# Optimization experiments

Hardware: AMD Instinct MI355X
Metric: run time of the kernel (lower is better)

The kernel has to match this reference:

```python
import jax, jax.numpy as jnp
import numpy as np
import math

EMBED = 1024
HEADS = 16
HEAD_DIM = EMBED // HEADS
FF = 4096
LAYERS = 4
BATCH = 2
SEQ = 2048
EPS = 1e-5
ADAPTIVE = True
MAX_LENGTH = 2048


def setup_inputs() -> dict:
    key = jax.random.key(0)
    ks = jax.random.split(key, 20)
    s = 0.02
    inp = {
        "x": jax.random.normal(ks[0], (BATCH, SEQ, EMBED), jnp.float32),
        # per-layer stacked parameters, torch Linear convention W:[out,in]
        "Wq": jax.random.normal(ks[1], (LAYERS, EMBED, EMBED)) * s,
        "bq": jnp.zeros((LAYERS, EMBED)),
        "Wk": jax.random.normal(ks[2], (LAYERS, EMBED, EMBED)) * s,
        "bk": jnp.zeros((LAYERS, EMBED)),
        "Wv": jax.random.normal(ks[3], (LAYERS, EMBED, EMBED)) * s,
        "bv": jnp.zeros((LAYERS, EMBED)),
        "Wo": jax.random.normal(ks[4], (LAYERS, EMBED, EMBED)) * s,
        "bo": jnp.zeros((LAYERS, EMBED)),
        "W1": jax.random.normal(ks[5], (LAYERS, FF, EMBED)) * s,
        "b1": jnp.zeros((LAYERS, FF)),
        "W2": jax.random.normal(ks[6], (LAYERS, EMBED, FF)) * s,
        "b2": jnp.zeros((LAYERS, EMBED)),
        "g1": jnp.ones((LAYERS, EMBED)),
        "be1": jnp.zeros((LAYERS, EMBED)),
        "g2": jnp.ones((LAYERS, EMBED)),
        "be2": jnp.zeros((LAYERS, EMBED)),
    }
    return inp


def _layer_norm(x, g, b):
    mu = jnp.mean(x, axis=-1, keepdims=True)
    var = jnp.mean(jnp.square(x - mu), axis=-1, keepdims=True)
    return (x - mu) * jax.lax.rsqrt(var + EPS) * g + b


def _band_mask(seq_len):
    # adaptive, length-dependent sparse band: window ~ sqrt(seq_len)
    w = int(math.ceil(math.sqrt(seq_len))) if ADAPTIVE else MAX_LENGTH
    idx = jnp.arange(seq_len)
    return jnp.abs(idx[:, None] - idx[None, :]) <= w  # [S,S] bool


def _sparse_attn(x, Wq, bq, Wk, bk, Wv, bv, Wo, bo, band):
    B, S, E = x.shape
    def proj(W, b):
        return (x @ W.T + b).reshape(B, S, HEADS, HEAD_DIM)
    q = proj(Wq, bq)
    k = proj(Wk, bk)
    v = proj(Wv, bv)
    scores = jnp.einsum("bshd,bthd->bhst", q, k) / math.sqrt(HEAD_DIM)
    scores = jnp.where(band[None, None], scores, jnp.float32(-1e9))
    attn = jax.nn.softmax(scores, axis=-1)
    out = jnp.einsum("bhst,bthd->bshd", attn, v).reshape(B, S, E)
    return out @ Wo.T + bo


def reference(x, Wq, bq, Wk, bk, Wv, bv, Wo, bo, W1, b1, W2, b2, g1, be1, g2, be2):
    band = _band_mask(x.shape[1])
    for i in range(LAYERS):
        attn = _sparse_attn(x, Wq[i], bq[i], Wk[i], bk[i], Wv[i], bv[i],
                            Wo[i], bo[i], band)
        x = _layer_norm(x + attn, g1[i], be1[i])
        ff = jax.nn.relu(x @ W1[i].T + b1[i]) @ W2[i].T + b2[i]
        x = _layer_norm(x + ff, g2[i], be2[i])
    return x  # dropout is identity in eval mode
```

## Files before the change

### kernel.cpp

```cpp
#include <hip/hip_runtime.h>
#include <hip/hip_bf16.h>

using bf16 = __hip_bfloat16;
typedef __bf16 bf16x8v __attribute__((ext_vector_type(8)));
typedef __bf16 bf16x4v __attribute__((ext_vector_type(4)));
typedef float f32x4v __attribute__((ext_vector_type(4)));

#define EMBED 1024
#define FF_DIM 4096
#define NTOK 4096
#define SEQL 2048
#define HD 64
#define WBAND 46
#define LN_EPS 1e-5f

__device__ __forceinline__ void gload16(const bf16* g, bf16* l)
{
  __builtin_amdgcn_global_load_lds(
      (const __attribute__((address_space(1))) void*)g,
      (__attribute__((address_space(3))) void*)l, 16, 0, 0);
}

__global__ __launch_bounds__(256) void detect_dtype(
    const unsigned int* __restrict__ xw, int* __restrict__ flag)
{
  __shared__ int votes[256];
  int v = 0;
#pragma unroll
  for (int j = 0; j < 4; j++) {
    unsigned int w = xw[1 + threadIdx.x * 4 + j];
    unsigned int e = (w >> 7) & 0xFFu;
    v += (e == 0u || (e >= 0x58u && e <= 0x88u)) ? 1 : 0;
  }
  votes[threadIdx.x] = v;
  __syncthreads();
  if (threadIdx.x == 0) {
    int s = 0;
    for (int i = 0; i < 256; i++) s += votes[i];
    *flag = (s > 512) ? 1 : 0;
  }
}

__global__ __launch_bounds__(256) void cast_param(
    const void* __restrict__ src, bf16* __restrict__ dst, int n,
    const int* __restrict__ dflag)
{
  const int is_bf16 = *dflag;
  for (int i = blockIdx.x * 256 + threadIdx.x; i < n; i += gridDim.x * 256)
    dst[i] = is_bf16 ? ((const bf16*)src)[i] : (bf16)(((const float*)src)[i]);
}

__global__ __launch_bounds__(256) void cast_in(
    const void* __restrict__ x, float* __restrict__ xf,
    bf16* __restrict__ xb, int n, const int* __restrict__ dflag)
{
  const int is_bf16 = *dflag;
  const int i = blockIdx.x * 256 + threadIdx.x;
  if (i < n) {
    float v = is_bf16 ? (float)((const bf16*)x)[i] : ((const float*)x)[i];
    xf[i] = v;
    xb[i] = (bf16)v;
  }
}

__global__ __launch_bounds__(256) void cast_weights(
    const void* __restrict__ wq, const void* __restrict__ wk,
    const void* __restrict__ wv, const void* __restrict__ wo,
    const void* __restrict__ w1, const void* __restrict__ w2,
    size_t off_ee, size_t off_fe, bf16* __restrict__ dst,
    const int* __restrict__ dflag)
{
  const int is_bf16 = *dflag;
  const int c = blockIdx.x * 256 + threadIdx.x;
  const size_t i = (size_t)c * 8;
  const void* src;
  size_t si;
  if (i < 4194304) {
    const int t = (int)(i >> 20);
    src = (t == 0) ? wq : (t == 1) ? wk : (t == 2) ? wv : wo;
    si  = off_ee + (i & 1048575);
  } else if (i < 8388608) { src = w1; si = off_fe + (i - 4194304); }
  else                    { src = w2; si = off_fe + (i - 8388608); }
  bf16x8v o;
  if (is_bf16) {
    o = *reinterpret_cast<const bf16x8v*>((const bf16*)src + si);
  } else {
    f32x4v a = *reinterpret_cast<const f32x4v*>((const float*)src + si);
    f32x4v b = *reinterpret_cast<const f32x4v*>((const float*)src + si + 4);
#pragma unroll
    for (int j = 0; j < 4; j++) { o[j] = (__bf16)a[j]; o[j + 4] = (__bf16)b[j]; }
  }
  *reinterpret_cast<bf16x8v*>(dst + i) = o;
}

template<int EPI, int BN>
__device__ __forceinline__ void gemm_core(
    const bf16* __restrict__ A, const bf16* __restrict__ W,
    const bf16* __restrict__ bias, bf16* __restrict__ C,
    int N, int K, int row0, int col0W, int col0C)
{
  __shared__ __align__(16) bf16 lA[128 * 32];
  __shared__ __align__(16) bf16 lB[BN * 32];
  constexpr int NJ = BN / 32;

  const int tid  = threadIdx.x;
  const int wave = tid >> 6;
  const int lane = tid & 63;
  const int wr0  = (wave >> 1) * 64;
  const int wc0  = (wave & 1) * (BN / 2);

  f32x4v acc[4][NJ];
#pragma unroll
  for (int i = 0; i < 4; i++)
#pragma unroll
    for (int j = 0; j < NJ; j++) acc[i][j] = (f32x4v){0.f, 0.f, 0.f, 0.f};

  const int srow = wave * 16 + (lane >> 2);
  const int skc  = (lane & 3) * 8;
  const bf16* Ag = A + (size_t)(row0 + srow) * K + skc;
  const bf16* Bg;
  if constexpr (BN == 128) Bg = W + (size_t)(col0W + srow) * K + skc;
  else                     Bg = W + (size_t)(col0W + (tid >> 2)) * K + (size_t)(tid & 3) * 8;
  bf16* lAp = lA + tid * 8;
  bf16* lBp = lB + tid * 8;

  const int fr = lane & 15;
  const int q8 = (lane >> 4) * 8;

  for (int k0 = 0; k0 < K; k0 += 32) {
    __syncthreads();
    gload16(Ag + k0, lAp);
    gload16(Ag + (size_t)64 * K + k0, lAp + 2048);
    gload16(Bg + k0, lBp);
    if constexpr (BN == 128)
      gload16(Bg + (size_t)64 * K + k0, lBp + 2048);
    __syncthreads();

    bf16x8v af[4], bw[NJ];
#pragma unroll
    for (int i = 0; i < 4; i++)
      af[i] = *reinterpret_cast<const bf16x8v*>(&lA[(wr0 + i * 16 + fr) * 32 + q8]);
#pragma unroll
    for (int j = 0; j < NJ; j++)
      bw[j] = *reinterpret_cast<const bf16x8v*>(&lB[(wc0 + j * 16 + fr) * 32 + q8]);
#pragma unroll
    for (int i = 0; i < 4; i++)
#pragma unroll
      for (int j = 0; j < NJ; j++)
        acc[i][j] = __builtin_amdgcn_mfma_f32_16x16x32_bf16(af[i], bw[j], acc[i][j], 0, 0, 0);
  }

  const int quad = (lane >> 4) * 4;
#pragma unroll
  for (int j = 0; j < NJ; j++) {
    const int col = col0C + wc0 + j * 16 + fr;
    const float bvf = (float)bias[col];
#pragma unroll
    for (int i = 0; i < 4; i++) {
      const int r0 = row0 + wr0 + i * 16 + quad;
#pragma unroll
      for (int r = 0; r < 4; r++) {
        float v = acc[i][j][r] + bvf;
        if (EPI == 1) v = fmaxf(v, 0.f);
        C[(size_t)(r0 + r) * N + col] = (bf16)v;
      }
    }
  }
}

template<int EPI, int BN>
__global__ __launch_bounds__(256) void gemm_bt(
    const bf16* __restrict__ A, const bf16* __restrict__ W,
    const bf16* __restrict__ bias, bf16* __restrict__ C, int N, int K)
{
  gemm_core<EPI, BN>(A, W, bias, C, N, K,
                     blockIdx.x * 128, blockIdx.y * BN, blockIdx.y * BN);
}

__global__ __launch_bounds__(256) void gemm_qkv(
    const bf16* __restrict__ A, const bf16* __restrict__ Wqkv,
    const bf16* __restrict__ bq, const bf16* __restrict__ bk, const bf16* __restrict__ bv,
    bf16* __restrict__ Cq, bf16* __restrict__ Ck, bf16* __restrict__ Cv, int K)
{
  const int cg = blockIdx.y * 128;
  const int t  = cg >> 10;
  const bf16* bias = (t == 0) ? bq : (t == 1) ? bk : bv;
  bf16*       C    = (t == 0) ? Cq : (t == 1) ? Ck : Cv;
  gemm_core<0, 128>(A, Wqkv, bias, C, 1024, K,
                    blockIdx.x * 128, cg, cg & 1023);
}

#define SKI(t, d)  ((((t) * 64) + (d)) ^ (((t) & 7) << 3))
#define SVI(d, t)  ((((d) * 128) + (t)) ^ (((d) & 7) << 3))
#define SPI(q, c)  ((((q) * 128) + (c)) ^ (((q) & 7) << 3))
#define SSI(q, c)  ((((q) * 128) + (c)) ^ (((q) & 7) << 2))

__global__ __launch_bounds__(256) void attn_band(
    const bf16* __restrict__ Q, const bf16* __restrict__ Kp,
    const bf16* __restrict__ Vp, bf16* __restrict__ O)
{
  const int sblk = blockIdx.x;
  const int bh   = blockIdx.y;
  const int b    = bh >> 4;
  const int h    = bh & 15;
  const int s0   = sblk * 32;
  int tlo = s0 - WBAND;       if (tlo < 0) tlo = 0;
  int thi = s0 + 31 + WBAND;  if (thi > SEQL - 1) thi = SEQL - 1;
  const int L = thi - tlo + 1;

  __shared__ __align__(16) bf16  sQf[32 * 64];
  __shared__ __align__(16) bf16  sKf[128 * 64];
  __shared__ __align__(16) bf16  sVtf[64 * 128];
  __shared__ __align__(16) float sSf[32 * 128];
  __shared__ __align__(16) bf16  sPf[32 * 128];
  __shared__ float red1[32][8];
  __shared__ float red2[32][8];
  __shared__ float sInv[32];

  const int tid  = threadIdx.x;
  const int wave = tid >> 6;
  const int lane = tid & 63;
  const size_t base = ((size_t)b * SEQL) * EMBED + (size_t)h * HD;

  bf16x8v vz;
#pragma unroll
  for (int j = 0; j < 8; j++) vz[j] = (__bf16)0.f;

  {
    const int sl = tid >> 3, d0 = (tid & 7) * 8;
    *reinterpret_cast<bf16x8v*>(&sQf[SKI(sl, d0)]) =
        *reinterpret_cast<const bf16x8v*>(&Q[base + (size_t)(s0 + sl) * EMBED + d0]);
  }
  for (int i = tid; i < 128 * 8; i += 256) {
    const int tl = i >> 3, d0 = (i & 7) * 8;
    bf16x8v v = vz;
    if (tl < L)
      v = *reinterpret_cast<const bf16x8v*>(&Kp[base + (size_t)(tlo + tl) * EMBED + d0]);
    *reinterpret_cast<bf16x8v*>(&sKf[SKI(tl, d0)]) = v;
  }
  for (int i = tid; i < 128 * 8; i += 256) {
    const int tl = i & 127, d0 = ((i >> 7) & 7) * 8;
    bf16x8v v = vz;
    if (tl < L)
      v = *reinterpret_cast<const bf16x8v*>(&Vp[base + (size_t)(tlo + tl) * EMBED + d0]);
#pragma unroll
    for (int j = 0; j < 8; j++)
      sVtf[SVI(d0 + j, tl)] = reinterpret_cast<const bf16*>(&v)[j];
  }
  __syncthreads();

  const int fr   = lane & 15;
  const int q8   = (lane >> 4) * 8;
  const int quad = (lane >> 4) * 4;

  {
    f32x4v acc[2][2];
#pragma unroll
    for (int mi = 0; mi < 2; mi++)
#pragma unroll
      for (int nj = 0; nj < 2; nj++) acc[mi][nj] = (f32x4v){0.f, 0.f, 0.f, 0.f};
#pragma unroll
    for (int ks = 0; ks < 2; ks++) {
      bf16x8v a0 = *reinterpret_cast<const bf16x8v*>(&sQf[SKI(fr,      ks * 32 + q8)]);
      bf16x8v a1 = *reinterpret_cast<const bf16x8v*>(&sQf[SKI(16 + fr, ks * 32 + q8)]);
      bf16x8v b0 = *reinterpret_cast<const bf16x8v*>(&sKf[SKI((wave * 2    ) * 16 + fr, ks * 32 + q8)]);
      bf16x8v b1 = *reinterpret_cast<const bf16x8v*>(&sKf[SKI((wave * 2 + 1) * 16 + fr, ks * 32 + q8)]);
      acc[0][0] = __builtin_amdgcn_mfma_f32_16x16x32_bf16(a0, b0, acc[0][0], 0, 0, 0);
      acc[0][1] = __builtin_amdgcn_mfma_f32_16x16x32_bf16(a0, b1, acc[0][1], 0, 0, 0);
      acc[1][0] = __builtin_amdgcn_mfma_f32_16x16x32_bf16(a1, b0, acc[1][0], 0, 0, 0);
      acc[1][1] = __builtin_amdgcn_mfma_f32_16x16x32_bf16(a1, b1, acc[1][1], 0, 0, 0);
    }
#pragma unroll
    for (int nj = 0; nj < 2; nj++) {
      const int c = (wave * 2 + nj) * 16 + fr;
      const int t = tlo + c;
      const bool cvalid = (c < L);
#pragma unroll
      for (int mi = 0; mi < 2; mi++) {
#pragma unroll
        for (int r = 0; r < 4; r++) {
          const int row = mi * 16 + quad + r;
          int dd = (s0 + row) - t; if (dd < 0) dd = -dd;
          sSf[SSI(row, c)] = (cvalid && dd <= WBAND) ? acc[mi][nj][r] * 0.125f
                                                     : -1e30f;
        }
      }
    }
  }
  __syncthreads();

  const int sl   = tid & 31;
  const int part = tid >> 5;
  float pmax = -1e30f;
#pragma unroll
  for (int k = 0; k < 16; k++) pmax = fmaxf(pmax, sSf[SSI(sl, part + 8 * k)]);
  red1[sl][part] = pmax;
  __syncthreads();
  float rmax = red1[sl][0];
#pragma unroll
  for (int p = 1; p < 8; p++) rmax = fmaxf(rmax, red1[sl][p]);

  float psum = 0.f;
#pragma unroll
  for (int k = 0; k < 16; k++) {
    const int c = part + 8 * k;
    float e = __expf(sSf[SSI(sl, c)] - rmax);
    sPf[SPI(sl, c)] = (bf16)e;
    psum += e;
  }
  red2[sl][part] = psum;
  __syncthreads();
  float rsum = 0.f;
#pragma unroll
  for (int p = 0; p < 8; p++) rsum += red2[sl][p];
  if (part == 0) sInv[sl] = 1.f / rsum;
  __syncthreads();

  {
    const int mi = wave >> 1;
    const int nb = (wave & 1) * 2;
    f32x4v acc[2];
    acc[0] = (f32x4v){0.f, 0.f, 0.f, 0.f};
    acc[1] = (f32x4v){0.f, 0.f, 0.f, 0.f};
#pragma unroll
    for (int ks = 0; ks < 4; ks++) {
      bf16x8v a  = *reinterpret_cast<const bf16x8v*>(&sPf[SPI(mi * 16 + fr, ks * 32 + q8)]);
      bf16x8v b0 = *reinterpret_cast<const bf16x8v*>(&sVtf[SVI((nb    ) * 16 + fr, ks * 32 + q8)]);
      bf16x8v b1 = *reinterpret_cast<const bf16x8v*>(&sVtf[SVI((nb + 1) * 16 + fr, ks * 32 + q8)]);
      acc[0] = __builtin_amdgcn_mfma_f32_16x16x32_bf16(a, b0, acc[0], 0, 0, 0);
      acc[1] = __builtin_amdgcn_mfma_f32_16x16x32_bf16(a, b1, acc[1], 0, 0, 0);
    }
#pragma unroll
    for (int nj = 0; nj < 2; nj++) {
      const int d = (nb + nj) * 16 + fr;
#pragma unroll
      for (int r = 0; r < 4; r++) {
        const int row = mi * 16 + quad + r;
        O[base + (size_t)(s0 + row) * EMBED + d] = (bf16)(acc[nj][r] * sInv[row]);
      }
    }
  }
}

__global__ __launch_bounds__(256) void resid_ln(
    const float* xin, const bf16* __restrict__ y,
    const bf16* __restrict__ g, const bf16* __restrict__ be,
    float* xf_out, bf16* __restrict__ xb_out,
    void* __restrict__ final_out, const int* __restrict__ dflag)
{
  __shared__ float red1[4];
  __shared__ float red2[4];
  const int row = blockIdx.x;
  const int tid = threadIdx.x;
  const size_t base = (size_t)row * EMBED + (size_t)tid * 4;

  f32x4v  xv = *reinterpret_cast<const f32x4v*>(xin + base);
  bf16x4v yv = *reinterpret_cast<const bf16x4v*>(y + base);
  float v[4];
#pragma unroll
  for (int j = 0; j < 4; j++) v[j] = xv[j] + (float)yv[j];

  float s = v[0] + v[1] + v[2] + v[3];
#pragma unroll
  for (int off = 32; off > 0; off >>= 1) s += __shfl_down(s, off, 64);
  if ((tid & 63) == 0) red1[tid >> 6] = s;
  __syncthreads();
  const float mu = (red1[0] + red1[1] + red1[2] + red1[3]) * (1.f / EMBED);

  float sq = 0.f;
#pragma unroll
  for (int j = 0; j < 4; j++) { const float d = v[j] - mu; sq += d * d; }
#pragma unroll
  for (int off = 32; off > 0; off >>= 1) sq += __shfl_down(sq, off, 64);
  if ((tid & 63) == 0) red2[tid >> 6] = sq;
  __syncthreads();
  const float rstd = rsqrtf((red2[0] + red2[1] + red2[2] + red2[3]) * (1.f / EMBED) + LN_EPS);

  bf16x4v gv = *reinterpret_cast<const bf16x4v*>(g + (size_t)tid * 4);
  bf16x4v bv = *reinterpret_cast<const bf16x4v*>(be + (size_t)tid * 4);
  f32x4v of;
  bf16x4v ov;
#pragma unroll
  for (int j = 0; j < 4; j++) {
    of[j] = (v[j] - mu) * rstd * (float)gv[j] + (float)bv[j];
    ov[j] = (__bf16)of[j];
  }
  *reinterpret_cast<f32x4v*>(xf_out + base) = of;
  *reinterpret_cast<bf16x4v*>(xb_out + base) = ov;
  if (final_out) {
    if (*dflag)
      *reinterpret_cast<bf16x4v*>((bf16*)final_out + base) = ov;
    else
      *reinterpret_cast<f32x4v*>((float*)final_out + base) = of;
  }
}

extern "C" void kernel_launch(void* const* d_in, const int* in_sizes, int n_in,
                              void* d_out, int out_size, void* d_ws, size_t ws_size,
                              hipStream_t stream)
{
  char* ws = (char*)d_ws;
  const size_t MB = 1024 * 1024;
  int*   flag = (int*)ws;
  bf16*  pp   = (bf16*)(ws + 4096);
  float* xf   = (float*)(ws + 1 * MB);
  bf16*  xb   = (bf16*)(ws + 17 * MB);
  bf16*  q    = (bf16*)(ws + 25 * MB);
  bf16*  kk   = (bf16*)(ws + 33 * MB);
  bf16*  vv   = (bf16*)(ws + 41 * MB);
  bf16*  ao   = q;
  bf16*  hh   = (bf16*)(ws + 25 * MB);
  bf16*  y    = (bf16*)(ws + 57 * MB);
  bf16*  wbf  = (bf16*)(ws + 65 * MB);

  bf16* pbq = pp;            bf16* pbk = pp + 4096;  bf16* pbv = pp + 8192;
  bf16* pbo = pp + 12288;    bf16* pb1 = pp + 16384; bf16* pb2 = pp + 32768;
  bf16* pg1 = pp + 36864;    bf16* pe1 = pp + 40960;
  bf16* pg2 = pp + 45056;    bf16* pe2 = pp + 49152;

  detect_dtype<<<1, 256, 0, stream>>>((const unsigned int*)d_in[0], flag);

  cast_param<<<16, 256, 0, stream>>>(d_in[2],  pbq, 4096,  flag);
  cast_param<<<16, 256, 0, stream>>>(d_in[4],  pbk, 4096,  flag);
  cast_param<<<16, 256, 0, stream>>>(d_in[6],  pbv, 4096,  flag);
  cast_param<<<16, 256, 0, stream>>>(d_in[8],  pbo, 4096,  flag);
  cast_param<<<64, 256, 0, stream>>>(d_in[10], pb1, 16384, flag);
  cast_param<<<16, 256, 0, stream>>>(d_in[12], pb2, 4096,  flag);
  cast_param<<<16, 256, 0, stream>>>(d_in[13], pg1, 4096,  flag);
  cast_param<<<16, 256, 0, stream>>>(d_in[14], pe1, 4096,  flag);
  cast_param<<<16, 256, 0, stream>>>(d_in[15], pg2, 4096,  flag);
  cast_param<<<16, 256, 0, stream>>>(d_in[16], pe2, 4096,  flag);

  cast_in<<<dim3((NTOK * EMBED) / 256), 256, 0, stream>>>(
      d_in[0], xf, xb, NTOK * EMBED, flag);

  for (int l = 0; l < 4; l++) {
    cast_weights<<<6144, 256, 0, stream>>>(
        d_in[1], d_in[3], d_in[5], d_in[7], d_in[9], d_in[11],
        (size_t)l * 1048576, (size_t)l * 4194304, wbf, flag);

    gemm_qkv<<<dim3(32, 24), 256, 0, stream>>>(
        xb, wbf, pbq + l * 1024, pbk + l * 1024, pbv + l * 1024,
        q, kk, vv, EMBED);
    attn_band<<<dim3(SEQL / 32, 32), 256, 0, stream>>>(q, kk, vv, ao);
    gemm_bt<0, 64><<<dim3(32, 16), 256, 0, stream>>>(
        ao, wbf + 3 * 1048576, pbo + l * 1024, y, EMBED, EMBED);
    resid_ln<<<dim3(NTOK), 256, 0, stream>>>(xf, y, pg1 + l * 1024, pe1 + l * 1024, xf, xb, nullptr, flag);
    gemm_bt<1, 128><<<dim3(32, 32), 256, 0, stream>>>(
        xb, wbf + 4 * 1048576, pb1 + l * 4096, hh, FF_DIM, EMBED);
    gemm_bt<0, 64><<<dim3(32, 16), 256, 0, stream>>>(
        hh, wbf + 8 * 1048576, pb2 + l * 1024, y, EMBED, FF_DIM);
    resid_ln<<<dim3(NTOK), 256, 0, stream>>>(xf, y, pg2 + l * 1024, pe2 + l * 1024, xf, xb,
                                             l == 3 ? d_out : nullptr, flag);
  }
}
```

Before: 1.201 ms.

## Split-K the N=1024 output GEMMs into two partials summed in residual LayerNorm

```diff
diff --git a/kernel.cpp b/kernel.cpp
--- a/kernel.cpp
+++ b/kernel.cpp
@@ -97,7 +97,8 @@
 __device__ __forceinline__ void gemm_core(
     const bf16* __restrict__ A, const bf16* __restrict__ W,
     const bf16* __restrict__ bias, bf16* __restrict__ C,
-    int N, int K, int row0, int col0W, int col0C)
+    int N, int Kstride, int Kbeg, int Klen,
+    int row0, int col0W, int col0C)
 {
   __shared__ __align__(16) bf16 lA[128 * 32];
   __shared__ __align__(16) bf16 lB[BN * 32];
@@ -117,23 +118,25 @@
 
   const int srow = wave * 16 + (lane >> 2);
   const int skc  = (lane & 3) * 8;
-  const bf16* Ag = A + (size_t)(row0 + srow) * K + skc;
+  const bf16* Ag = A + (size_t)(row0 + srow) * Kstride + Kbeg + skc;
   const bf16* Bg;
-  if constexpr (BN == 128) Bg = W + (size_t)(col0W + srow) * K + skc;
-  else                     Bg = W + (size_t)(col0W + (tid >> 2)) * K + (size_t)(tid & 3) * 8;
+  if constexpr (BN == 128)
+    Bg = W + (size_t)(col0W + srow) * Kstride + Kbeg + skc;
+  else
+    Bg = W + (size_t)(col0W + (tid >> 2)) * Kstride + Kbeg + (size_t)(tid & 3) * 8;
   bf16* lAp = lA + tid * 8;
   bf16* lBp = lB + tid * 8;
 
   const int fr = lane & 15;
   const int q8 = (lane >> 4) * 8;
 
-  for (int k0 = 0; k0 < K; k0 += 32) {
+  for (int k0 = 0; k0 < Klen; k0 += 32) {
     __syncthreads();
     gload16(Ag + k0, lAp);
-    gload16(Ag + (size_t)64 * K + k0, lAp + 2048);
+    gload16(Ag + (size_t)64 * Kstride + k0, lAp + 2048);
     gload16(Bg + k0, lBp);
     if constexpr (BN == 128)
-      gload16(Bg + (size_t)64 * K + k0, lBp + 2048);
+      gload16(Bg + (size_t)64 * Kstride + k0, lBp + 2048);
     __syncthreads();
 
     bf16x8v af[4], bw[NJ];
@@ -154,7 +157,7 @@
 #pragma unroll
   for (int j = 0; j < NJ; j++) {
     const int col = col0C + wc0 + j * 16 + fr;
-    const float bvf = (float)bias[col];
+    const float bvf = bias ? (float)bias[col] : 0.f;
 #pragma unroll
     for (int i = 0; i < 4; i++) {
       const int r0 = row0 + wr0 + i * 16 + quad;
@@ -168,12 +171,16 @@
   }
 }
 
-template<int EPI, int BN>
+template<int EPI, int BN, int NS>
 __global__ __launch_bounds__(256) void gemm_bt(
     const bf16* __restrict__ A, const bf16* __restrict__ W,
-    const bf16* __restrict__ bias, bf16* __restrict__ C, int N, int K)
-{
-  gemm_core<EPI, BN>(A, W, bias, C, N, K,
+    const bf16* __restrict__ bias, bf16* __restrict__ C0, bf16* __restrict__ C1,
+    int N, int K)
+{
+  const int z  = (NS > 1) ? blockIdx.z : 0;
+  const int Kp = K / NS;
+  gemm_core<EPI, BN>(A, W, z == 0 ? bias : nullptr, z == 0 ? C0 : C1,
+                     N, K, z * Kp, Kp,
                      blockIdx.x * 128, blockIdx.y * BN, blockIdx.y * BN);
 }
 
@@ -186,7 +193,7 @@
   const int t  = cg >> 10;
   const bf16* bias = (t == 0) ? bq : (t == 1) ? bk : bv;
   bf16*       C    = (t == 0) ? Cq : (t == 1) ? Ck : Cv;
-  gemm_core<0, 128>(A, Wqkv, bias, C, 1024, K,
+  gemm_core<0, 128>(A, Wqkv, bias, C, 1024, K, 0, K,
                     blockIdx.x * 128, cg, cg & 1023);
 }
 
@@ -343,9 +350,9 @@
 }
 
 __global__ __launch_bounds__(256) void resid_ln(
-    const float* xin, const bf16* __restrict__ y,
+    const float* xin, const bf16* __restrict__ y0, const bf16* y1,
     const bf16* __restrict__ g, const bf16* __restrict__ be,
-    float* xf_out, bf16* __restrict__ xb_out,
+    float* xf_out, bf16* xb_out,
     void* __restrict__ final_out, const int* __restrict__ dflag)
 {
   __shared__ float red1[4];
@@ -354,11 +361,12 @@
   const int tid = threadIdx.x;
   const size_t base = (size_t)row * EMBED + (size_t)tid * 4;
 
-  f32x4v  xv = *reinterpret_cast<const f32x4v*>(xin + base);
-  bf16x4v yv = *reinterpret_cast<const bf16x4v*>(y + base);
+  f32x4v  xv  = *reinterpret_cast<const f32x4v*>(xin + base);
+  bf16x4v yv0 = *reinterpret_cast<const bf16x4v*>(y0 + base);
+  bf16x4v yv1 = *reinterpret_cast<const bf16x4v*>(y1 + base);
   float v[4];
 #pragma unroll
-  for (int j = 0; j < 4; j++) v[j] = xv[j] + (float)yv[j];
+  for (int j = 0; j < 4; j++) v[j] = xv[j] + (float)yv0[j] + (float)yv1[j];
 
   float s = v[0] + v[1] + v[2] + v[3];
 #pragma unroll
@@ -443,14 +451,16 @@
         xb, wbf, pbq + l * 1024, pbk + l * 1024, pbv + l * 1024,
         q, kk, vv, EMBED);
     attn_band<<<dim3(SEQL / 32, 32), 256, 0, stream>>>(q, kk, vv, ao);
-    gemm_bt<0, 64><<<dim3(32, 16), 256, 0, stream>>>(
-        ao, wbf + 3 * 1048576, pbo + l * 1024, y, EMBED, EMBED);
-    resid_ln<<<dim3(NTOK), 256, 0, stream>>>(xf, y, pg1 + l * 1024, pe1 + l * 1024, xf, xb, nullptr, flag);
-    gemm_bt<1, 128><<<dim3(32, 32), 256, 0, stream>>>(
-        xb, wbf + 4 * 1048576, pb1 + l * 4096, hh, FF_DIM, EMBED);
-    gemm_bt<0, 64><<<dim3(32, 16), 256, 0, stream>>>(
-        hh, wbf + 8 * 1048576, pb2 + l * 1024, y, EMBED, FF_DIM);
-    resid_ln<<<dim3(NTOK), 256, 0, stream>>>(xf, y, pg2 + l * 1024, pe2 + l * 1024, xf, xb,
-                                             l == 3 ? d_out : nullptr, flag);
-  }
-}
+    gemm_bt<0, 64, 2><<<dim3(32, 16, 2), 256, 0, stream>>>(
+        ao, wbf + 3 * 1048576, pbo + l * 1024, kk, vv, EMBED, EMBED);
+    resid_ln<<<dim3(NTOK), 256, 0, stream>>>(
+        xf, kk, vv, pg1 + l * 1024, pe1 + l * 1024, xf, xb, nullptr, flag);
+    gemm_bt<1, 128, 1><<<dim3(32, 32, 1), 256, 0, stream>>>(
+        xb, wbf + 4 * 1048576, pb1 + l * 4096, hh, nullptr, FF_DIM, EMBED);
+    gemm_bt<0, 64, 2><<<dim3(32, 16, 2), 256, 0, stream>>>(
+        hh, wbf + 8 * 1048576, pb2 + l * 1024, y, xb, EMBED, FF_DIM);
+    resid_ln<<<dim3(NTOK), 256, 0, stream>>>(
+        xf, y, xb, pg2 + l * 1024, pe2 + l * 1024, xf, xb,
+        l == 3 ? d_out : nullptr, flag);
+  }
+}
```

Result: faster. 1.132 ms (-5.7%).
